# Performance work log

Hardware: AMD Instinct MI355X
Metric: run time of the kernel (lower is better)

The kernel has to match this reference:

```python
import math
import jax, jax.numpy as jnp
import numpy as np

B, L, C_S, C_Z, H, C, PQK, PV = 1, 768, 256, 128, 8, 32, 4, 8
OUT_DIM = H * C + H * PV * 3 + H * PV + H * 4  # 544
EPS_LN = 1e-5


def _ln(x, w, b):
    m = jnp.mean(x, axis=-1, keepdims=True)
    v = jnp.mean((x - m) ** 2, axis=-1, keepdims=True)
    return (x - m) * jax.lax.rsqrt(v + EPS_LN) * w + b


def setup_inputs() -> dict:
    key = jax.random.key(0)
    ks = jax.random.split(key, 16)
    f = lambda k, shape, s=1.0: jax.random.normal(k, shape, jnp.float32) * s
    w = 0.05  # weight init scale
    return {
        "s": f(ks[0], (B, L, C_S)),
        "z": f(ks[1], (B, L, L, C_Z)),
        "R": f(ks[2], (B, L, 3, 3)),
        "t": f(ks[3], (B, L, 3)),
        "mask": jnp.ones((B, L), jnp.float32),
        "ln_s_w": jnp.ones((C_S,), jnp.float32),
        "ln_s_b": jnp.zeros((C_S,), jnp.float32),
        "ln_z_w": jnp.ones((C_Z,), jnp.float32),
        "ln_z_b": jnp.zeros((C_Z,), jnp.float32),
        "Wq": f(ks[4], (C_S, H * C), w),
        "Wk": f(ks[5], (C_S, H * C), w),
        "Wv": f(ks[6], (C_S, H * C), w),
        "W_pair_bias": f(ks[7], (C_Z, H), w),
        "Wq_pts": f(ks[8], (C_S, H * PQK * 3), w),
        "Wk_pts": f(ks[9], (C_S, H * PQK * 3), w),
        "Wv_pts": f(ks[10], (C_S, H * PV * 3), w),
        "point_weights": f(ks[11], (H,), 0.1),
        "W_pair_out": f(ks[12], (C_Z, H * 4), w),
        "W_out": f(ks[13], (OUT_DIM, C_S), w),
        "b_out": jnp.zeros((C_S,), jnp.float32),
    }


def reference(s, z, R, t, mask, ln_s_w, ln_s_b, ln_z_w, ln_z_b,
              Wq, Wk, Wv, W_pair_bias, Wq_pts, Wk_pts, Wv_pts,
              point_weights, W_pair_out, W_out, b_out):
    s = _ln(s, ln_s_w, ln_s_b)               # [B,L,c_s]
    z = _ln(z, ln_z_w, ln_z_b)               # [B,L,L,c_z]

    q = (s @ Wq).reshape(B, L, H, C)
    k = (s @ Wk).reshape(B, L, H, C)
    v = (s @ Wv).reshape(B, L, H, C)

    scalar_logits = jnp.einsum('bihc,bjhc->bhij', q, k) / math.sqrt(C)
    pair_bias = jnp.transpose(z @ W_pair_bias, (0, 3, 1, 2))  # [B,H,L,L]

    q_pts = (s @ Wq_pts).reshape(B, L, H, PQK, 3)
    k_pts = (s @ Wk_pts).reshape(B, L, H, PQK, 3)
    v_pts = (s @ Wv_pts).reshape(B, L, H, PV, 3)

    t_b = t[:, :, None, None, :]
    apply_T = lambda p: jnp.einsum('blxy,blhpy->blhpx', R, p) + t_b
    q_pts_g = apply_T(q_pts)  # [B,L,H,Pqk,3]
    k_pts_g = apply_T(k_pts)
    v_pts_g = apply_T(v_pts)  # [B,L,H,Pv,3]

    diff = q_pts_g[:, :, None] - k_pts_g[:, None]          # [B,L,L,H,P,3]
    sq_dist = jnp.sum(diff ** 2, axis=(-1, -2))            # [B,L,L,H]
    sq_dist = jnp.transpose(sq_dist, (0, 3, 1, 2))         # [B,H,L,L]

    pw = jax.nn.softplus(point_weights)[None, :, None, None]
    logits = scalar_logits + pair_bias - 0.5 * pw * sq_dist

    pair_mask = mask[:, :, None] * mask[:, None, :]
    logits = jnp.where(pair_mask[:, None] == 0, -1e9, logits)
    attn = jax.nn.softmax(logits, axis=-1)                 # [B,H,L,L]

    scalar_out = jnp.einsum('bhij,bjhc->bihc', attn, v).reshape(B, L, H * C)

    pair_v = (z @ W_pair_out).reshape(B, L, L, H, 4)
    pair_out = jnp.einsum('bhij,bijhd->bihd', attn, pair_v).reshape(B, L, H * 4)

    pt_out_g = jnp.einsum('bhij,bjhpc->bihpc', attn, v_pts_g)    # [B,L,H,Pv,3]
    # invert transform: R^T (x - t)
    pt_out_l = jnp.einsum('blxy,blhpx->blhpy', R, pt_out_g - t_b)
    point_out = pt_out_l.reshape(B, L, H * PV * 3)
    point_norms = jnp.sqrt(jnp.sum(pt_out_l ** 2, axis=-1) + 1e-8).reshape(B, L, H * PV)

    s_update = jnp.concatenate([scalar_out, point_out, point_norms, pair_out], axis=-1)
    s_update = s_update @ W_out + b_out
    s_update = s_update * mask[:, :, None]
    return s_update, attn
```

## Files before the change

kernel.cpp:

```cpp
#include <hip/hip_runtime.h>
#include <math.h>

#define L 768
#define CS 256
#define CZ 128
#define H 8
#define LL (L*L)

typedef __attribute__((ext_vector_type(8))) short bf16x8;
typedef __attribute__((ext_vector_type(4))) float floatx4;

static __device__ __forceinline__ unsigned short f2bf(float f){
  unsigned int u = __float_as_uint(f);
  unsigned int r = (u + 0x7fffu + ((u >> 16) & 1u)) >> 16;
  return (unsigned short)r;
}

__global__ void k_ln_s(const float* __restrict__ s, const float* __restrict__ w,
                       const float* __restrict__ b, float* __restrict__ out) {
  int i = blockIdx.x, t = threadIdx.x;
  __shared__ float red[256];
  float x = s[i*CS + t];
  red[t] = x; __syncthreads();
  for (int s2=128; s2>0; s2>>=1){ if (t<s2) red[t]+=red[t+s2]; __syncthreads(); }
  float mean = red[0] * (1.0f/CS); __syncthreads();
  float d = x - mean;
  red[t] = d*d; __syncthreads();
  for (int s2=128; s2>0; s2>>=1){ if (t<s2) red[t]+=red[t+s2]; __syncthreads(); }
  float var = red[0] * (1.0f/CS);
  float rstd = rsqrtf(var + 1e-5f);
  out[i*CS+t] = d*rstd*w[t] + b[t];
}

__global__ void k_proj(const float* __restrict__ s_n,
                       const float* __restrict__ Wq, const float* __restrict__ Wk, const float* __restrict__ Wv,
                       const float* __restrict__ Wqp, const float* __restrict__ Wkp, const float* __restrict__ Wvp,
                       const float* __restrict__ R, const float* __restrict__ t,
                       float* __restrict__ q, float* __restrict__ kT, float* __restrict__ v,
                       float* __restrict__ qpg, float* __restrict__ kpgT, float* __restrict__ vpg) {
  int i0 = blockIdx.x*2, tid = threadIdx.x;
  __shared__ float srow[2][256];
  __shared__ float qraw[2][96], kraw[2][96], vraw[2][192];
  __shared__ float Rl[2][9], tl[2][3];
  srow[0][tid] = s_n[i0*CS + tid];
  srow[1][tid] = s_n[(i0+1)*CS + tid];
  if (tid < 18) Rl[tid/9][tid%9] = R[i0*9 + tid];
  if (tid >= 24 && tid < 30) tl[(tid-24)/3][(tid-24)%3] = t[i0*3 + (tid-24)];
  __syncthreads();
  float aq0=0.f, ak0=0.f, av0=0.f, aq1=0.f, ak1=0.f, av1=0.f;
  #pragma unroll 4
  for (int c=0;c<256;c++){
    float s0=srow[0][c], s1=srow[1][c];
    float wq=Wq[c*256+tid], wk=Wk[c*256+tid], wv=Wv[c*256+tid];
    aq0=fmaf(s0,wq,aq0); aq1=fmaf(s1,wq,aq1);
    ak0=fmaf(s0,wk,ak0); ak1=fmaf(s1,wk,ak1);
    av0=fmaf(s0,wv,av0); av1=fmaf(s1,wv,av1);
  }
  q[i0*256+tid]=aq0; q[(i0+1)*256+tid]=aq1;
  kT[(size_t)tid*L + i0]=ak0; kT[(size_t)tid*L + i0+1]=ak1;
  v[i0*256+tid]=av0; v[(i0+1)*256+tid]=av1;
  if (tid < 96){
    float a10=0.f,a20=0.f,a11=0.f,a21=0.f;
    #pragma unroll 4
    for (int c=0;c<256;c++){
      float s0=srow[0][c], s1=srow[1][c];
      float w1=Wqp[c*96+tid], w2=Wkp[c*96+tid];
      a10=fmaf(s0,w1,a10); a11=fmaf(s1,w1,a11);
      a20=fmaf(s0,w2,a20); a21=fmaf(s1,w2,a21);
    }
    qraw[0][tid]=a10; qraw[1][tid]=a11; kraw[0][tid]=a20; kraw[1][tid]=a21;
  }
  if (tid < 192){
    float a30=0.f,a31=0.f;
    #pragma unroll 4
    for (int c=0;c<256;c++){
      float w3=Wvp[c*192+tid];
      a30=fmaf(srow[0][c],w3,a30); a31=fmaf(srow[1][c],w3,a31);
    }
    vraw[0][tid]=a30; vraw[1][tid]=a31;
  }
  __syncthreads();
  #pragma unroll
  for (int rr=0; rr<2; rr++){
    int i = i0 + rr;
    if (tid < 32){
      int b0 = tid*3;
      float px=qraw[rr][b0], py=qraw[rr][b0+1], pz=qraw[rr][b0+2];
      #pragma unroll
      for (int x=0;x<3;x++)
        qpg[i*96 + b0 + x] = Rl[rr][x*3]*px + Rl[rr][x*3+1]*py + Rl[rr][x*3+2]*pz + tl[rr][x];
    } else if (tid < 64){
      int b0 = (tid-32)*3;
      float px=kraw[rr][b0], py=kraw[rr][b0+1], pz=kraw[rr][b0+2];
      #pragma unroll
      for (int x=0;x<3;x++)
        kpgT[(size_t)(b0+x)*L + i] = Rl[rr][x*3]*px + Rl[rr][x*3+1]*py + Rl[rr][x*3+2]*pz + tl[rr][x];
    } else if (tid < 128){
      int b0 = (tid-64)*3;
      float px=vraw[rr][b0], py=vraw[rr][b0+1], pz=vraw[rr][b0+2];
      #pragma unroll
      for (int x=0;x<3;x++)
        vpg[i*192 + b0 + x] = Rl[rr][x*3]*px + Rl[rr][x*3+1]*py + Rl[rr][x*3+2]*pz + tl[rr][x];
    }
  }
}

__global__ void k_prep(const float* __restrict__ lzw, const float* __restrict__ lzb,
                       const float* __restrict__ Wpb, const float* __restrict__ Wpo,
                       unsigned short* __restrict__ Bpack, float* __restrict__ uv) {
  int tid = threadIdx.x;
  if (tid < 48){
    int o = tid;
    float uo = 0.f, vo = 0.f;
    for (int c=0;c<128;c++){
      float W = (o<8) ? Wpb[c*8+o] : ((o<40) ? Wpo[c*32+o-8] : 0.f);
      uo = fmaf(lzw[c], W, uo);
      vo = fmaf(lzb[c], W, vo);
    }
    uv[o] = uo; uv[48+o] = vo;
  }
  for (int idx=tid; idx<6144; idx+=256){
    int jj = idx & 7, lane = (idx>>3)&63, kb = (idx>>9)&3, nt = idx>>11;
    int c = kb*32 + (lane>>4)*8 + jj;
    int o = nt*16 + (lane&15);
    float W = (o<8) ? Wpb[c*8+o] : ((o<40) ? Wpo[c*32+o-8] : 0.f);
    Bpack[idx] = f2bf(lzw[c]*W);
  }
}

__global__ __launch_bounds__(256) void k_zfuse(
    const float* __restrict__ z, const unsigned short* __restrict__ Bpack,
    const float* __restrict__ uv, float* __restrict__ pb, float* __restrict__ pv) {
  int i = blockIdx.x, jt = blockIdx.y, tid = threadIdx.x;
  int j0 = jt * 128;
  __shared__ unsigned short znb[128*136];
  __shared__ float smean[128], srstd[128];

  int lane = tid & 63;
  const bf16x8* Bp = (const bf16x8*)Bpack;
  bf16x8 bfr[3][4];
  #pragma unroll
  for (int nt=0; nt<3; nt++)
    #pragma unroll
    for (int kb=0; kb<4; kb++)
      bfr[nt][kb] = Bp[(nt*4+kb)*64 + lane];

  int row = tid >> 1, sub = tid & 1;
  const float4* zrow = (const float4*)(z + ((size_t)i*L + j0 + row)*CZ);
  float sm = 0.f, sq = 0.f;
  #pragma unroll 8
  for (int kk=0; kk<16; kk++){
    float4 v4 = zrow[sub + 2*kk];
    sm += (v4.x+v4.y)+(v4.z+v4.w);
    sq = fmaf(v4.x,v4.x, fmaf(v4.y,v4.y, fmaf(v4.z,v4.z, fmaf(v4.w,v4.w, sq))));
    ushort4 pk = make_ushort4(f2bf(v4.x), f2bf(v4.y), f2bf(v4.z), f2bf(v4.w));
    *(ushort4*)&znb[row*136 + (sub+2*kk)*4] = pk;
  }
  sm += __shfl_xor(sm,1); sq += __shfl_xor(sq,1);
  if (sub == 0){
    float mean = sm*(1.f/128.f);
    float var  = sq*(1.f/128.f) - mean*mean;
    smean[row] = mean; srstd[row] = rsqrtf(var + 1e-5f);
  }

  int w = tid >> 6;
  int n16 = lane & 15, quad = lane >> 4;
  #pragma unroll
  for (int mt2=0; mt2<2; mt2++){
    int mt = w*2 + mt2;
    floatx4 acc0 = {0,0,0,0}, acc1 = {0,0,0,0}, acc2 = {0,0,0,0};
    #pragma unroll
    for (int kb=0; kb<4; kb++){
      bf16x8 afrag = *(const bf16x8*)&znb[(mt*16 + n16)*136 + kb*32 + quad*8];
      acc0 = __builtin_amdgcn_mfma_f32_16x16x32_bf16(afrag, bfr[0][kb], acc0, 0,0,0);
      acc1 = __builtin_amdgcn_mfma_f32_16x16x32_bf16(afrag, bfr[1][kb], acc1, 0,0,0);
      acc2 = __builtin_amdgcn_mfma_f32_16x16x32_bf16(afrag, bfr[2][kb], acc2, 0,0,0);
    }
    #pragma unroll
    for (int nt=0; nt<3; nt++){
      int o = nt*16 + n16;
      if (o >= 40) continue;
      float uo = uv[o], vo = uv[48+o];
      const floatx4 acc = (nt==0) ? acc0 : (nt==1) ? acc1 : acc2;
      #pragma unroll
      for (int reg=0; reg<4; reg++){
        int jl = mt*16 + quad*4 + reg;
        int j = j0 + jl;
        float val = srstd[jl]*(acc[reg] - smean[jl]*uo) + vo;
        if (o < 8) pb[(size_t)o*LL + (size_t)i*L + j] = val;
        else       pv[((size_t)i*L + j)*32 + (o-8)] = val;
      }
    }
  }
}

__global__ __launch_bounds__(256) void k_attn_fused(
    const float* __restrict__ q, const float* __restrict__ kT, const float* __restrict__ v,
    const float* __restrict__ qpg, const float* __restrict__ kpgT, const float* __restrict__ vpg,
    float* __restrict__ pb_attn, const float* __restrict__ pv,
    const float* __restrict__ R, const float* __restrict__ t,
    const float* __restrict__ point_weights, const float* __restrict__ mask,
    float* __restrict__ su_pre) {
  int i = blockIdx.x, tid = threadIdx.x;
  int h = tid >> 5, jl = tid & 31;

  __shared__ float sml[8*776];
  __shared__ float sm_q[256];
  __shared__ float sm_qp[96];
  __shared__ float sm_mask[768];
  __shared__ float sm_ptg[192];
  __shared__ float sm_ptl[192];
  __shared__ float Rl[9], tl[3];

  sm_q[tid] = q[i*256 + tid];
  if (tid < 96) sm_qp[tid] = qpg[i*96 + tid];
  if (tid >= 96 && tid < 105) Rl[tid-96] = R[i*9 + (tid-96)];
  if (tid >= 112 && tid < 115) tl[tid-112] = t[i*3 + (tid-112)];
  #pragma unroll
  for (int rr=0; rr<3; rr++) sm_mask[rr*256 + tid] = mask[rr*256 + tid];
  __syncthreads();

  float pw = log1pf(__expf(point_weights[h]));
  float mi = mask[i];
  float qreg[32];
  #pragma unroll
  for (int c=0;c<32;c++) qreg[c] = sm_q[h*32+c];
  float qp_reg[12];
  #pragma unroll
  for (int pc=0;pc<12;pc++) qp_reg[pc] = sm_qp[h*12+pc];

  const float* kTb  = kT  + (size_t)(h*32)*L + jl;
  const float* kpTb = kpgT + (size_t)(h*12)*L + jl;
  const float* pbb  = pb_attn + (size_t)h*LL + (size_t)i*L + jl;

  float lg[24];
  for (int jt=0; jt<24; jt++){
    int joff = jt*32;
    float dot = 0.f;
    #pragma unroll
    for (int c=0;c<32;c++) dot = fmaf(qreg[c], kTb[(size_t)c*L + joff], dot);
    float sq = 0.f;
    #pragma unroll
    for (int pc=0;pc<12;pc++){ float d = qp_reg[pc] - kpTb[(size_t)pc*L + joff]; sq = fmaf(d,d,sq); }
    float lgv = dot*0.17677669529663687f + pbb[joff] - 0.5f*pw*sq;
    if (mi*sm_mask[joff+jl] == 0.f) lgv = -1e9f;
    lg[jt] = lgv;
  }

  float m = -1e30f;
  #pragma unroll
  for (int jt=0; jt<24; jt++) m = fmaxf(m, lg[jt]);
  #pragma unroll
  for (int d=1; d<32; d<<=1) m = fmaxf(m, __shfl_xor(m, d));
  float ssum = 0.f;
  #pragma unroll
  for (int jt=0; jt<24; jt++){ float e = __expf(lg[jt]-m); lg[jt]=e; ssum+=e; }
  #pragma unroll
  for (int d=1; d<32; d<<=1) ssum += __shfl_xor(ssum, d);
  float inv = 1.0f/ssum;
  float* pbw = pb_attn + (size_t)h*LL + (size_t)i*L + jl;
  #pragma unroll
  for (int jt=0; jt<24; jt++){
    float a = lg[jt]*inv;
    sml[h*776 + jt*32 + jl] = a;
    pbw[jt*32] = a;
  }
  __syncthreads();

  const float2* src; int str; const float* smlB;
  if (tid < 128)      { src = (const float2*)v + tid;                         str = 128; smlB = sml + (tid>>4)*776; }
  else if (tid < 224) { int e2=(tid-128)*2; src = (const float2*)vpg + (tid-128); str = 96; smlB = sml + (e2/24)*776; }
  else if (tid < 240) { int e2=(tid-224)*2; src = (const float2*)(pv + (size_t)i*L*32) + (tid-224); str = 16; smlB = sml + (e2>>2)*776; }
  else                { src = (const float2*)v; str = 0; smlB = sml; }
  float2 acc = {0.f, 0.f};
  #pragma unroll 8
  for (int j=0; j<768; j++){
    float a = smlB[j];
    float2 vv = src[(size_t)j*str];
    acc.x = fmaf(a, vv.x, acc.x);
    acc.y = fmaf(a, vv.y, acc.y);
  }
  if (tid < 128)      *(float2*)&su_pre[i*544 + tid*2] = acc;
  else if (tid < 224) { int e2=(tid-128)*2; sm_ptg[e2] = acc.x; sm_ptg[e2+1] = acc.y; }
  else if (tid < 240) *(float2*)&su_pre[i*544 + 512 + (tid-224)*2] = acc;
  __syncthreads();

  if (tid < 192){
    int hh = tid/24, rem = tid%24, p = rem/3, y = rem%3;
    float lv = 0.f;
    #pragma unroll
    for (int x=0;x<3;x++) lv = fmaf(Rl[x*3+y], sm_ptg[hh*24+p*3+x]-tl[x], lv);
    sm_ptl[tid] = lv;
    su_pre[i*544 + 256 + tid] = lv;
  }
  __syncthreads();
  if (tid < 64){
    float a0=sm_ptl[tid*3], a1=sm_ptl[tid*3+1], a2=sm_ptl[tid*3+2];
    su_pre[i*544 + 448 + tid] = sqrtf(a0*a0+a1*a1+a2*a2 + 1e-8f);
  }
}

__global__ void k_out(const float* __restrict__ su_pre, const float* __restrict__ W_out,
                      const float* __restrict__ b_out, const float* __restrict__ mask,
                      float* __restrict__ out) {
  int i = blockIdx.x, tid = threadIdx.x;
  __shared__ float srow[544];
  for (int idx=tid; idx<544; idx+=256) srow[idx] = su_pre[i*544+idx];
  __syncthreads();
  float acc = b_out[tid];
  #pragma unroll 4
  for (int c=0;c<544;c++) acc = fmaf(srow[c], W_out[c*256+tid], acc);
  out[i*256+tid] = acc * mask[i];
}

extern "C" void kernel_launch(void* const* d_in, const int* in_sizes, int n_in,
                              void* d_out, int out_size, void* d_ws, size_t ws_size,
                              hipStream_t stream) {
  const float* s    = (const float*)d_in[0];
  const float* z    = (const float*)d_in[1];
  const float* R    = (const float*)d_in[2];
  const float* t    = (const float*)d_in[3];
  const float* mask = (const float*)d_in[4];
  const float* lsw  = (const float*)d_in[5];
  const float* lsb  = (const float*)d_in[6];
  const float* lzw  = (const float*)d_in[7];
  const float* lzb  = (const float*)d_in[8];
  const float* Wq   = (const float*)d_in[9];
  const float* Wk   = (const float*)d_in[10];
  const float* Wv   = (const float*)d_in[11];
  const float* Wpb  = (const float*)d_in[12];
  const float* Wqp  = (const float*)d_in[13];
  const float* Wkp  = (const float*)d_in[14];
  const float* Wvp  = (const float*)d_in[15];
  const float* pwts = (const float*)d_in[16];
  const float* Wpo  = (const float*)d_in[17];
  const float* Wout = (const float*)d_in[18];
  const float* bout = (const float*)d_in[19];

  float* out0 = (float*)d_out;
  float* attn = out0 + (size_t)L*CS;

  float* ws   = (float*)d_ws;
  float* s_n  = ws;                        size_t off = (size_t)L*CS;
  float* q    = ws + off;                  off += (size_t)L*CS;
  float* kT   = ws + off;                  off += (size_t)L*CS;
  float* v    = ws + off;                  off += (size_t)L*CS;
  float* qpg  = ws + off;                  off += (size_t)L*96;
  float* kpgT = ws + off;                  off += (size_t)L*96;
  float* vpg  = ws + off;                  off += (size_t)L*192;
  float* pv   = ws + off;                  off += (size_t)LL*32;
  float* su   = ws + off;                  off += (size_t)L*544;
  unsigned short* Bpack = (unsigned short*)(ws + off); off += 3072;
  float* uv   = ws + off;                  off += 96;

  k_prep<<<1, 256, 0, stream>>>(lzw, lzb, Wpb, Wpo, Bpack, uv);
  k_ln_s<<<L, 256, 0, stream>>>(s, lsw, lsb, s_n);
  k_proj<<<L/2, 256, 0, stream>>>(s_n, Wq, Wk, Wv, Wqp, Wkp, Wvp, R, t,
                                  q, kT, v, qpg, kpgT, vpg);
  k_zfuse<<<dim3(L, L/128), 256, 0, stream>>>(z, Bpack, uv, attn, pv);
  k_attn_fused<<<L, 256, 0, stream>>>(q, kT, v, qpg, kpgT, vpg, attn, pv,
                                      R, t, pwts, mask, su);
  k_out<<<L, 256, 0, stream>>>(su, Wout, bout, mask, out0);
}
```

Baseline: 777.2 us.

## Store pair values in bf16 and restructure attention to one warp per row-head

The pair-value tensor is now written in bf16 with a head-major layout, which halves the largest intermediate write and read. The attention kernel is reorganised so each 32-thread group handles one (row, head) pair across a 2D grid. Each thread covers 4 contiguous keys using float4 loads, and the value accumulation is reduced with warp shuffles instead of a shared-memory split across threads. Weight packing in k_prep is spread over 25 blocks. The bf16 rounding of the pair values adds a small precision loss, and the many shuffle reductions raise register pressure.

```diff
diff --git a/kernel.cpp b/kernel.cpp
--- a/kernel.cpp
+++ b/kernel.cpp
@@ -14,6 +14,9 @@
   unsigned int u = __float_as_uint(f);
   unsigned int r = (u + 0x7fffu + ((u >> 16) & 1u)) >> 16;
   return (unsigned short)r;
+}
+static __device__ __forceinline__ float bf2f(unsigned short u){
+  return __uint_as_float(((unsigned int)u) << 16);
 }
 
 __global__ void k_ln_s(const float* __restrict__ s, const float* __restrict__ w,
@@ -108,29 +111,31 @@
 __global__ void k_prep(const float* __restrict__ lzw, const float* __restrict__ lzb,
                        const float* __restrict__ Wpb, const float* __restrict__ Wpo,
                        unsigned short* __restrict__ Bpack, float* __restrict__ uv) {
-  int tid = threadIdx.x;
-  if (tid < 48){
-    int o = tid;
-    float uo = 0.f, vo = 0.f;
-    for (int c=0;c<128;c++){
-      float W = (o<8) ? Wpb[c*8+o] : ((o<40) ? Wpo[c*32+o-8] : 0.f);
-      uo = fmaf(lzw[c], W, uo);
-      vo = fmaf(lzb[c], W, vo);
-    }
-    uv[o] = uo; uv[48+o] = vo;
-  }
-  for (int idx=tid; idx<6144; idx+=256){
-    int jj = idx & 7, lane = (idx>>3)&63, kb = (idx>>9)&3, nt = idx>>11;
-    int c = kb*32 + (lane>>4)*8 + jj;
-    int o = nt*16 + (lane&15);
-    float W = (o<8) ? Wpb[c*8+o] : ((o<40) ? Wpo[c*32+o-8] : 0.f);
-    Bpack[idx] = f2bf(lzw[c]*W);
-  }
+  int tid = threadIdx.x, bx = blockIdx.x;
+  if (bx == 0){
+    if (tid < 48){
+      int o = tid;
+      float uo = 0.f, vo = 0.f;
+      for (int c=0;c<128;c++){
+        float W = (o<8) ? Wpb[c*8+o] : ((o<40) ? Wpo[c*32+o-8] : 0.f);
+        uo = fmaf(lzw[c], W, uo);
+        vo = fmaf(lzb[c], W, vo);
+      }
+      uv[o] = uo; uv[48+o] = vo;
+    }
+    return;
+  }
+  int idx = (bx-1)*256 + tid;
+  int jj = idx & 7, lane = (idx>>3)&63, kb = (idx>>9)&3, nt = idx>>11;
+  int c = kb*32 + (lane>>4)*8 + jj;
+  int o = nt*16 + (lane&15);
+  float W = (o<8) ? Wpb[c*8+o] : ((o<40) ? Wpo[c*32+o-8] : 0.f);
+  Bpack[idx] = f2bf(lzw[c]*W);
 }
 
 __global__ __launch_bounds__(256) void k_zfuse(
     const float* __restrict__ z, const unsigned short* __restrict__ Bpack,
-    const float* __restrict__ uv, float* __restrict__ pb, float* __restrict__ pv) {
+    const float* __restrict__ uv, float* __restrict__ pb, unsigned short* __restrict__ pvb) {
   int i = blockIdx.x, jt = blockIdx.y, tid = threadIdx.x;
   int j0 = jt * 128;
   __shared__ unsigned short znb[128*136];
@@ -188,115 +193,192 @@
         int j = j0 + jl;
         float val = srstd[jl]*(acc[reg] - smean[jl]*uo) + vo;
         if (o < 8) pb[(size_t)o*LL + (size_t)i*L + j] = val;
-        else       pv[((size_t)i*L + j)*32 + (o-8)] = val;
+        else {
+          int oo = o - 8;
+          pvb[(size_t)(oo>>2)*LL*4 + ((size_t)i*L + j)*4 + (oo&3)] = f2bf(val);
+        }
       }
     }
   }
 }
 
-__global__ __launch_bounds__(256) void k_attn_fused(
+__global__ __launch_bounds__(256) void k_attn2(
     const float* __restrict__ q, const float* __restrict__ kT, const float* __restrict__ v,
     const float* __restrict__ qpg, const float* __restrict__ kpgT, const float* __restrict__ vpg,
-    float* __restrict__ pb_attn, const float* __restrict__ pv,
+    float* __restrict__ attn, const unsigned short* __restrict__ pvb,
     const float* __restrict__ R, const float* __restrict__ t,
     const float* __restrict__ point_weights, const float* __restrict__ mask,
-    float* __restrict__ su_pre) {
-  int i = blockIdx.x, tid = threadIdx.x;
-  int h = tid >> 5, jl = tid & 31;
-
-  __shared__ float sml[8*776];
-  __shared__ float sm_q[256];
-  __shared__ float sm_qp[96];
-  __shared__ float sm_mask[768];
-  __shared__ float sm_ptg[192];
-  __shared__ float sm_ptl[192];
-  __shared__ float Rl[9], tl[3];
-
-  sm_q[tid] = q[i*256 + tid];
-  if (tid < 96) sm_qp[tid] = qpg[i*96 + tid];
-  if (tid >= 96 && tid < 105) Rl[tid-96] = R[i*9 + (tid-96)];
-  if (tid >= 112 && tid < 115) tl[tid-112] = t[i*3 + (tid-112)];
-  #pragma unroll
-  for (int rr=0; rr<3; rr++) sm_mask[rr*256 + tid] = mask[rr*256 + tid];
-  __syncthreads();
-
-  float pw = log1pf(__expf(point_weights[h]));
-  float mi = mask[i];
+    float* __restrict__ su) {
+  const int h  = blockIdx.y;
+  const int i  = blockIdx.x*8 + (threadIdx.x >> 5);
+  const int jg = threadIdx.x & 31;
+
+  const float pw = log1pf(__expf(point_weights[h]));
+  const float mi = mask[i];
+
   float qreg[32];
-  #pragma unroll
-  for (int c=0;c<32;c++) qreg[c] = sm_q[h*32+c];
-  float qp_reg[12];
-  #pragma unroll
-  for (int pc=0;pc<12;pc++) qp_reg[pc] = sm_qp[h*12+pc];
-
-  const float* kTb  = kT  + (size_t)(h*32)*L + jl;
-  const float* kpTb = kpgT + (size_t)(h*12)*L + jl;
-  const float* pbb  = pb_attn + (size_t)h*LL + (size_t)i*L + jl;
-
-  float lg[24];
-  for (int jt=0; jt<24; jt++){
-    int joff = jt*32;
-    float dot = 0.f;
-    #pragma unroll
-    for (int c=0;c<32;c++) dot = fmaf(qreg[c], kTb[(size_t)c*L + joff], dot);
-    float sq = 0.f;
-    #pragma unroll
-    for (int pc=0;pc<12;pc++){ float d = qp_reg[pc] - kpTb[(size_t)pc*L + joff]; sq = fmaf(d,d,sq); }
-    float lgv = dot*0.17677669529663687f + pbb[joff] - 0.5f*pw*sq;
-    if (mi*sm_mask[joff+jl] == 0.f) lgv = -1e9f;
-    lg[jt] = lgv;
+  {
+    const float4* qr = (const float4*)(q + (size_t)i*256 + h*32);
+    #pragma unroll
+    for (int c4=0;c4<8;c4++){
+      float4 t4 = qr[c4];
+      qreg[c4*4+0]=t4.x; qreg[c4*4+1]=t4.y; qreg[c4*4+2]=t4.z; qreg[c4*4+3]=t4.w;
+    }
+  }
+  float qp[12];
+  {
+    const float4* qr = (const float4*)(qpg + (size_t)i*96 + h*12);
+    #pragma unroll
+    for (int c4=0;c4<3;c4++){
+      float4 t4 = qr[c4];
+      qp[c4*4+0]=t4.x; qp[c4*4+1]=t4.y; qp[c4*4+2]=t4.z; qp[c4*4+3]=t4.w;
+    }
+  }
+
+  const float* kbase  = kT   + (size_t)(h*32)*L + jg*4;
+  const float* kpbase = kpgT + (size_t)(h*12)*L + jg*4;
+  float* pbrow = attn + (size_t)h*LL + (size_t)i*L + jg*4;
+
+  float lgr[24];
+  #pragma unroll
+  for (int jt=0; jt<6; jt++){
+    const int j0 = jt*128;
+    float d0=0.f,d1=0.f,d2=0.f,d3=0.f;
+    #pragma unroll
+    for (int c=0;c<32;c++){
+      float4 kv = *(const float4*)(kbase + (size_t)c*L + j0);
+      float qc = qreg[c];
+      d0 = fmaf(qc, kv.x, d0); d1 = fmaf(qc, kv.y, d1);
+      d2 = fmaf(qc, kv.z, d2); d3 = fmaf(qc, kv.w, d3);
+    }
+    float s0=0.f,s1=0.f,s2=0.f,s3=0.f;
+    #pragma unroll
+    for (int pc=0;pc<12;pc++){
+      float4 kv = *(const float4*)(kpbase + (size_t)pc*L + j0);
+      float qc = qp[pc];
+      float e0=qc-kv.x, e1=qc-kv.y, e2=qc-kv.z, e3=qc-kv.w;
+      s0=fmaf(e0,e0,s0); s1=fmaf(e1,e1,s1); s2=fmaf(e2,e2,s2); s3=fmaf(e3,e3,s3);
+    }
+    float4 pb4 = *(const float4*)(pbrow + j0);
+    float4 mk4 = *(const float4*)(mask + j0 + jg*4);
+    const float SCL = 0.17677669529663687f;
+    float l0 = fmaf(d0,SCL,pb4.x) - 0.5f*pw*s0;
+    float l1 = fmaf(d1,SCL,pb4.y) - 0.5f*pw*s1;
+    float l2 = fmaf(d2,SCL,pb4.z) - 0.5f*pw*s2;
+    float l3 = fmaf(d3,SCL,pb4.w) - 0.5f*pw*s3;
+    if (mi*mk4.x == 0.f) l0 = -1e9f;
+    if (mi*mk4.y == 0.f) l1 = -1e9f;
+    if (mi*mk4.z == 0.f) l2 = -1e9f;
+    if (mi*mk4.w == 0.f) l3 = -1e9f;
+    lgr[jt*4+0]=l0; lgr[jt*4+1]=l1; lgr[jt*4+2]=l2; lgr[jt*4+3]=l3;
   }
 
   float m = -1e30f;
   #pragma unroll
-  for (int jt=0; jt<24; jt++) m = fmaxf(m, lg[jt]);
+  for (int u=0;u<24;u++) m = fmaxf(m, lgr[u]);
   #pragma unroll
   for (int d=1; d<32; d<<=1) m = fmaxf(m, __shfl_xor(m, d));
-  float ssum = 0.f;
-  #pragma unroll
-  for (int jt=0; jt<24; jt++){ float e = __expf(lg[jt]-m); lg[jt]=e; ssum+=e; }
-  #pragma unroll
-  for (int d=1; d<32; d<<=1) ssum += __shfl_xor(ssum, d);
-  float inv = 1.0f/ssum;
-  float* pbw = pb_attn + (size_t)h*LL + (size_t)i*L + jl;
-  #pragma unroll
-  for (int jt=0; jt<24; jt++){
-    float a = lg[jt]*inv;
-    sml[h*776 + jt*32 + jl] = a;
-    pbw[jt*32] = a;
-  }
-  __syncthreads();
-
-  const float2* src; int str; const float* smlB;
-  if (tid < 128)      { src = (const float2*)v + tid;                         str = 128; smlB = sml + (tid>>4)*776; }
-  else if (tid < 224) { int e2=(tid-128)*2; src = (const float2*)vpg + (tid-128); str = 96; smlB = sml + (e2/24)*776; }
-  else if (tid < 240) { int e2=(tid-224)*2; src = (const float2*)(pv + (size_t)i*L*32) + (tid-224); str = 16; smlB = sml + (e2>>2)*776; }
-  else                { src = (const float2*)v; str = 0; smlB = sml; }
-  float2 acc = {0.f, 0.f};
-  #pragma unroll 8
-  for (int j=0; j<768; j++){
-    float a = smlB[j];
-    float2 vv = src[(size_t)j*str];
-    acc.x = fmaf(a, vv.x, acc.x);
-    acc.y = fmaf(a, vv.y, acc.y);
-  }
-  if (tid < 128)      *(float2*)&su_pre[i*544 + tid*2] = acc;
-  else if (tid < 224) { int e2=(tid-128)*2; sm_ptg[e2] = acc.x; sm_ptg[e2+1] = acc.y; }
-  else if (tid < 240) *(float2*)&su_pre[i*544 + 512 + (tid-224)*2] = acc;
-  __syncthreads();
-
-  if (tid < 192){
-    int hh = tid/24, rem = tid%24, p = rem/3, y = rem%3;
-    float lv = 0.f;
-    #pragma unroll
-    for (int x=0;x<3;x++) lv = fmaf(Rl[x*3+y], sm_ptg[hh*24+p*3+x]-tl[x], lv);
-    sm_ptl[tid] = lv;
-    su_pre[i*544 + 256 + tid] = lv;
-  }
-  __syncthreads();
-  if (tid < 64){
-    float a0=sm_ptl[tid*3], a1=sm_ptl[tid*3+1], a2=sm_ptl[tid*3+2];
-    su_pre[i*544 + 448 + tid] = sqrtf(a0*a0+a1*a1+a2*a2 + 1e-8f);
+  float ss = 0.f;
+  #pragma unroll
+  for (int u=0;u<24;u++){ float e = __expf(lgr[u]-m); lgr[u]=e; ss+=e; }
+  #pragma unroll
+  for (int d=1; d<32; d<<=1) ss += __shfl_xor(ss, d);
+  float inv = 1.0f/ss;
+  #pragma unroll
+  for (int u=0;u<24;u++) lgr[u] *= inv;
+  #pragma unroll
+  for (int jt=0;jt<6;jt++){
+    float4 a4;
+    a4.x=lgr[jt*4+0]; a4.y=lgr[jt*4+1]; a4.z=lgr[jt*4+2]; a4.w=lgr[jt*4+3];
+    *(float4*)(pbrow + jt*128) = a4;
+  }
+
+  float4 accv[8], accp[6], accq;
+  #pragma unroll
+  for (int c4=0;c4<8;c4++){ accv[c4].x=0.f; accv[c4].y=0.f; accv[c4].z=0.f; accv[c4].w=0.f; }
+  #pragma unroll
+  for (int c4=0;c4<6;c4++){ accp[c4].x=0.f; accp[c4].y=0.f; accp[c4].z=0.f; accp[c4].w=0.f; }
+  accq.x=0.f; accq.y=0.f; accq.z=0.f; accq.w=0.f;
+
+  const unsigned short* pvrow = pvb + (size_t)h*LL*4 + (size_t)i*L*4;
+  #pragma unroll
+  for (int jt=0;jt<6;jt++){
+    #pragma unroll
+    for (int r=0;r<4;r++){
+      const int j = jt*128 + jg*4 + r;
+      const float a = lgr[jt*4+r];
+      const float4* vr = (const float4*)(v + (size_t)j*256 + h*32);
+      #pragma unroll
+      for (int c4=0;c4<8;c4++){
+        float4 vv = vr[c4];
+        accv[c4].x = fmaf(a, vv.x, accv[c4].x);
+        accv[c4].y = fmaf(a, vv.y, accv[c4].y);
+        accv[c4].z = fmaf(a, vv.z, accv[c4].z);
+        accv[c4].w = fmaf(a, vv.w, accv[c4].w);
+      }
+      const float4* pr = (const float4*)(vpg + (size_t)j*192 + h*24);
+      #pragma unroll
+      for (int c4=0;c4<6;c4++){
+        float4 vv = pr[c4];
+        accp[c4].x = fmaf(a, vv.x, accp[c4].x);
+        accp[c4].y = fmaf(a, vv.y, accp[c4].y);
+        accp[c4].z = fmaf(a, vv.z, accp[c4].z);
+        accp[c4].w = fmaf(a, vv.w, accp[c4].w);
+      }
+      ushort4 pk = *(const ushort4*)(pvrow + (size_t)j*4);
+      accq.x = fmaf(a, bf2f(pk.x), accq.x);
+      accq.y = fmaf(a, bf2f(pk.y), accq.y);
+      accq.z = fmaf(a, bf2f(pk.z), accq.z);
+      accq.w = fmaf(a, bf2f(pk.w), accq.w);
+    }
+  }
+
+  #pragma unroll
+  for (int d=1; d<32; d<<=1){
+    #pragma unroll
+    for (int c4=0;c4<8;c4++){
+      accv[c4].x += __shfl_xor(accv[c4].x,d); accv[c4].y += __shfl_xor(accv[c4].y,d);
+      accv[c4].z += __shfl_xor(accv[c4].z,d); accv[c4].w += __shfl_xor(accv[c4].w,d);
+    }
+    #pragma unroll
+    for (int c4=0;c4<6;c4++){
+      accp[c4].x += __shfl_xor(accp[c4].x,d); accp[c4].y += __shfl_xor(accp[c4].y,d);
+      accp[c4].z += __shfl_xor(accp[c4].z,d); accp[c4].w += __shfl_xor(accp[c4].w,d);
+    }
+    accq.x += __shfl_xor(accq.x,d); accq.y += __shfl_xor(accq.y,d);
+    accq.z += __shfl_xor(accq.z,d); accq.w += __shfl_xor(accq.w,d);
+  }
+
+  if (jg == 0){
+    float* so = su + (size_t)i*544;
+    float4* s4 = (float4*)(so + h*32);
+    #pragma unroll
+    for (int c4=0;c4<8;c4++) s4[c4] = accv[c4];
+
+    float Rl[9], tl[3];
+    #pragma unroll
+    for (int x=0;x<9;x++) Rl[x] = R[i*9+x];
+    tl[0]=t[i*3]; tl[1]=t[i*3+1]; tl[2]=t[i*3+2];
+    float pg[24];
+    #pragma unroll
+    for (int c4=0;c4<6;c4++){
+      pg[c4*4+0]=accp[c4].x; pg[c4*4+1]=accp[c4].y; pg[c4*4+2]=accp[c4].z; pg[c4*4+3]=accp[c4].w;
+    }
+    float lv[24];
+    #pragma unroll
+    for (int p=0;p<8;p++){
+      float gx = pg[p*3+0]-tl[0], gy = pg[p*3+1]-tl[1], gz = pg[p*3+2]-tl[2];
+      #pragma unroll
+      for (int y=0;y<3;y++)
+        lv[p*3+y] = Rl[y]*gx + Rl[3+y]*gy + Rl[6+y]*gz;
+    }
+    #pragma unroll
+    for (int k=0;k<24;k++) so[256 + h*24 + k] = lv[k];
+    #pragma unroll
+    for (int p=0;p<8;p++)
+      so[448 + h*8 + p] = sqrtf(lv[p*3]*lv[p*3] + lv[p*3+1]*lv[p*3+1] + lv[p*3+2]*lv[p*3+2] + 1e-8f);
+    so[512 + h*4 + 0] = accq.x; so[512 + h*4 + 1] = accq.y;
+    so[512 + h*4 + 2] = accq.z; so[512 + h*4 + 3] = accq.w;
   }
 }
 
@@ -348,17 +430,17 @@
   float* qpg  = ws + off;                  off += (size_t)L*96;
   float* kpgT = ws + off;                  off += (size_t)L*96;
   float* vpg  = ws + off;                  off += (size_t)L*192;
-  float* pv   = ws + off;                  off += (size_t)LL*32;
+  unsigned short* pvb = (unsigned short*)(ws + off); off += (size_t)LL*16;
   float* su   = ws + off;                  off += (size_t)L*544;
   unsigned short* Bpack = (unsigned short*)(ws + off); off += 3072;
   float* uv   = ws + off;                  off += 96;
 
-  k_prep<<<1, 256, 0, stream>>>(lzw, lzb, Wpb, Wpo, Bpack, uv);
+  k_prep<<<25, 256, 0, stream>>>(lzw, lzb, Wpb, Wpo, Bpack, uv);
   k_ln_s<<<L, 256, 0, stream>>>(s, lsw, lsb, s_n);
   k_proj<<<L/2, 256, 0, stream>>>(s_n, Wq, Wk, Wv, Wqp, Wkp, Wvp, R, t,
                                   q, kT, v, qpg, kpgT, vpg);
-  k_zfuse<<<dim3(L, L/128), 256, 0, stream>>>(z, Bpack, uv, attn, pv);
-  k_attn_fused<<<L, 256, 0, stream>>>(q, kT, v, qpg, kpgT, vpg, attn, pv,
-                                      R, t, pwts, mask, su);
+  k_zfuse<<<dim3(L, L/128), 256, 0, stream>>>(z, Bpack, uv, attn, pvb);
+  k_attn2<<<dim3(L/8, H), 256, 0, stream>>>(q, kT, v, qpg, kpgT, vpg, attn, pvb,
+                                            R, t, pwts, mask, su);
   k_out<<<L, 256, 0, stream>>>(su, Wout, bout, mask, out0);
 }
```

Result: slower. 881.1 us (+13.4%).
